# Kernel tuning notes

Measured on AMD Instinct MI355X. Metric: run time of the kernel, lower is better.

The kernel has to match this reference:

```python
import jax, jax.numpy as jnp
import numpy as np


def setup_inputs() -> dict:
    key = jax.random.key(0)
    ks = jax.random.split(key, 6)
    B, n_tok, n_RoI = 8, 64, 100
    T_hidden, I_hidden = 768, 1024
    P = I_hidden // 2  # projection = 512
    s_q = 1.0 / np.sqrt(T_hidden)
    s_k = 1.0 / np.sqrt(I_hidden)
    s_w = 1.0 / np.sqrt(P)
    return {
        "encT": jax.random.normal(ks[0], (B, n_tok, T_hidden), jnp.float32),
        "encI": jax.random.normal(ks[1], (B, n_RoI, I_hidden), jnp.float32),
        "mask": jnp.zeros((B, 1, n_tok, n_RoI), jnp.float32),
        "Wq": jax.random.normal(ks[2], (T_hidden, P), jnp.float32) * s_q,
        "bq": jnp.zeros((P,), jnp.float32),
        "Wk": jax.random.normal(ks[3], (I_hidden, P), jnp.float32) * s_k,
        "bk": jnp.zeros((P,), jnp.float32),
        "w": jax.random.normal(ks[4], (P,), jnp.float32) * s_w,
        "b": jnp.zeros((1,), jnp.float32),
    }


def reference(encT, encI, mask, Wq, bq, Wk, bk, w, b):
    # Q_mlp / K_mlp: Linear + exact GELU (torch nn.GELU default)
    q = jax.nn.gelu(jnp.einsum('bth,hp->btp', encT, Wq) + bq, approximate=False)  # [B,T,P]
    k = jax.nn.gelu(jnp.einsum('brh,hp->brp', encI, Wk) + bk, approximate=False)  # [B,R,P]
    # broadcast add (instead of repeat/view), tanh, then Linear(P,1)
    fusion = jnp.tanh(q[:, :, None, :] + k[:, None, :, :])  # [B,T,R,P]
    logits = jnp.einsum('btrp,p->btr', fusion, w) + b[0]      # [B,T,R]
    return logits + jnp.squeeze(mask, axis=1)
```

## Files before the change

### kernel.cpp

```cpp
#include <hip/hip_runtime.h>
#include <math.h>

#define B_  8
#define T_  64
#define R_  100
#define TH_ 768
#define IH_ 1024
#define P_  512
#define N_  512

#define CTANH 2.88539008177792681f

typedef short short8  __attribute__((ext_vector_type(8)));
typedef float floatx4 __attribute__((ext_vector_type(4)));

__device__ __forceinline__ ushort f2bf(float f) {
  union { float f; unsigned int u; } v; v.f = f;
  unsigned int r = v.u + 0x7FFFu + ((v.u >> 16) & 1u);
  return (ushort)(r >> 16);
}

#define PADK 40

__global__ __launch_bounds__(256) void mfma_linear_gelu(
    const float* __restrict__ encT, const float* __restrict__ Wq,
    const float* __restrict__ bq, float* __restrict__ qout,
    const float* __restrict__ encI, const float* __restrict__ Wk,
    const float* __restrict__ bk, float* __restrict__ kout) {
  const int rt = blockIdx.y;
  const bool isQ = rt < 8;
  const float* __restrict__ X = isQ ? encT : encI;
  const float* __restrict__ W = isQ ? Wq : Wk;
  const float* __restrict__ bias = isQ ? bq : bk;
  float* __restrict__ Y = isQ ? qout : kout;
  const int M    = isQ ? (B_ * T_) : (B_ * R_);
  const int KDIM = isQ ? TH_ : IH_;
  const int row0 = (isQ ? rt : (rt - 8)) * 64;
  const int col0 = blockIdx.x * 64;
  const int ntiles = KDIM / 32;

  __shared__ ushort As[64 * PADK];
  __shared__ ushort Bs[64 * PADK];

  const int tid = threadIdx.x;

  const int arow = tid >> 2;
  const int akq  = (tid & 3) * 8;
  const int arowc = min(row0 + arow, M - 1);
  const float* __restrict__ Xp = X + (size_t)arowc * KDIM + akq;

  const int bkp = (tid >> 4) * 2;
  const int bn4 = (tid & 15) * 4;
  const float* __restrict__ Wp = W + (size_t)bkp * N_ + col0 + bn4;

  const int wave = tid >> 6;
  const int lane = tid & 63;
  const int wm = (wave >> 1) * 32;
  const int wn = (wave & 1) * 32;
  const int l15 = lane & 15;
  const int q8  = (lane >> 4) * 8;

  floatx4 acc00 = {0.f,0.f,0.f,0.f}, acc01 = {0.f,0.f,0.f,0.f};
  floatx4 acc10 = {0.f,0.f,0.f,0.f}, acc11 = {0.f,0.f,0.f,0.f};

  float4 a0 = *(const float4*)(Xp + 0);
  float4 a1 = *(const float4*)(Xp + 4);
  float4 b0 = *(const float4*)(Wp);
  float4 b1 = *(const float4*)(Wp + N_);

  for (int kt = 0; kt < ntiles; ++kt) {
    {
      short8 pk;
      pk[0] = (short)f2bf(a0.x); pk[1] = (short)f2bf(a0.y);
      pk[2] = (short)f2bf(a0.z); pk[3] = (short)f2bf(a0.w);
      pk[4] = (short)f2bf(a1.x); pk[5] = (short)f2bf(a1.y);
      pk[6] = (short)f2bf(a1.z); pk[7] = (short)f2bf(a1.w);
      *(short8*)&As[arow * PADK + akq] = pk;
    }
    {
      unsigned int p0 = (unsigned int)f2bf(b0.x) | ((unsigned int)f2bf(b1.x) << 16);
      unsigned int p1 = (unsigned int)f2bf(b0.y) | ((unsigned int)f2bf(b1.y) << 16);
      unsigned int p2 = (unsigned int)f2bf(b0.z) | ((unsigned int)f2bf(b1.z) << 16);
      unsigned int p3 = (unsigned int)f2bf(b0.w) | ((unsigned int)f2bf(b1.w) << 16);
      *(unsigned int*)&Bs[(bn4 + 0) * PADK + bkp] = p0;
      *(unsigned int*)&Bs[(bn4 + 1) * PADK + bkp] = p1;
      *(unsigned int*)&Bs[(bn4 + 2) * PADK + bkp] = p2;
      *(unsigned int*)&Bs[(bn4 + 3) * PADK + bkp] = p3;
    }
    __syncthreads();

    if (kt + 1 < ntiles) {
      const int kb = (kt + 1) * 32;
      a0 = *(const float4*)(Xp + kb);
      a1 = *(const float4*)(Xp + kb + 4);
      b0 = *(const float4*)(W + (size_t)(kb + bkp) * N_ + col0 + bn4);
      b1 = *(const float4*)(W + (size_t)(kb + bkp + 1) * N_ + col0 + bn4);
    }

    short8 af0 = *(const short8*)&As[(wm + l15) * PADK + q8];
    short8 af1 = *(const short8*)&As[(wm + 16 + l15) * PADK + q8];
    short8 bf0 = *(const short8*)&Bs[(wn + l15) * PADK + q8];
    short8 bf1 = *(const short8*)&Bs[(wn + 16 + l15) * PADK + q8];
    acc00 = __builtin_amdgcn_mfma_f32_16x16x32_bf16(af0, bf0, acc00, 0, 0, 0);
    acc01 = __builtin_amdgcn_mfma_f32_16x16x32_bf16(af0, bf1, acc01, 0, 0, 0);
    acc10 = __builtin_amdgcn_mfma_f32_16x16x32_bf16(af1, bf0, acc10, 0, 0, 0);
    acc11 = __builtin_amdgcn_mfma_f32_16x16x32_bf16(af1, bf1, acc11, 0, 0, 0);
    __syncthreads();
  }

  const float is2 = 0.70710678118654752f;
  const float bia0 = bias[col0 + wn + l15];
  const float bia1 = bias[col0 + wn + 16 + l15];
  const int rbase = row0 + wm + (lane >> 4) * 4;

  #pragma unroll
  for (int r = 0; r < 4; ++r) {
    int row = rbase + r;
    if (row < M) {
      float v0 = acc00[r] + bia0;
      Y[(size_t)row * N_ + col0 + wn + l15] =
          CTANH * 0.5f * v0 * (1.f + erff(v0 * is2));
      float v1 = acc01[r] + bia1;
      Y[(size_t)row * N_ + col0 + wn + 16 + l15] =
          CTANH * 0.5f * v1 * (1.f + erff(v1 * is2));
    }
    int row2 = rbase + 16 + r;
    if (row2 < M) {
      float v2 = acc10[r] + bia0;
      Y[(size_t)row2 * N_ + col0 + wn + l15] =
          CTANH * 0.5f * v2 * (1.f + erff(v2 * is2));
      float v3 = acc11[r] + bia1;
      Y[(size_t)row2 * N_ + col0 + wn + 16 + l15] =
          CTANH * 0.5f * v3 * (1.f + erff(v3 * is2));
    }
  }
}

__global__ __launch_bounds__(256) void fuse_kernel(
    const float* __restrict__ q, const float* __restrict__ k,
    const float* __restrict__ w, const float* __restrict__ bscalar,
    const float* __restrict__ mask, float* __restrict__ out) {
  const int bt = blockIdx.x;
  const int wave = threadIdx.x >> 6;
  const int rg = blockIdx.y * 4 + wave;
  if (rg >= 25) return;
  const int lane = threadIdx.x & 63;
  const int sub  = lane >> 4;
  const int pi   = lane & 15;
  const int r = rg * 4 + sub;
  const int b = bt >> 6;

  const float* __restrict__ qp = q + (size_t)bt * P_ + pi * 4;
  const float* __restrict__ kp = k + (size_t)(b * R_ + r) * P_ + pi * 4;
  const float* __restrict__ wp = w + pi * 4;

  float acc0 = 0.f, acc1 = 0.f;
  #pragma unroll
  for (int i = 0; i < 8; ++i) {
    float4 qv = *(const float4*)(qp + i * 64);
    float4 kv = *(const float4*)(kp + i * 64);
    float4 wv = *(const float4*)(wp + i * 64);
    float x, e, d, s;
    x = qv.x + kv.x;
    e = __builtin_amdgcn_exp2f(x);
    d = __builtin_amdgcn_rcpf(1.f + e);
    s = fmaf(-2.f, d, 1.f);
    acc0 = fmaf(wv.x, s, acc0);
    x = qv.y + kv.y;
    e = __builtin_amdgcn_exp2f(x);
    d = __builtin_amdgcn_rcpf(1.f + e);
    s = fmaf(-2.f, d, 1.f);
    acc1 = fmaf(wv.y, s, acc1);
    x = qv.z + kv.z;
    e = __builtin_amdgcn_exp2f(x);
    d = __builtin_amdgcn_rcpf(1.f + e);
    s = fmaf(-2.f, d, 1.f);
    acc0 = fmaf(wv.z, s, acc0);
    x = qv.w + kv.w;
    e = __builtin_amdgcn_exp2f(x);
    d = __builtin_amdgcn_rcpf(1.f + e);
    s = fmaf(-2.f, d, 1.f);
    acc1 = fmaf(wv.w, s, acc1);
  }
  float acc = acc0 + acc1;
  #pragma unroll
  for (int off = 1; off < 16; off <<= 1) acc += __shfl_xor(acc, off, 64);

  if (pi == 0) {
    out[(size_t)bt * R_ + r] = acc + bscalar[0] + mask[(size_t)bt * R_ + r];
  }
}

extern "C" void kernel_launch(void* const* d_in, const int* in_sizes, int n_in,
                              void* d_out, int out_size, void* d_ws, size_t ws_size,
                              hipStream_t stream) {
  const float* encT = (const float*)d_in[0];
  const float* encI = (const float*)d_in[1];
  const float* mask = (const float*)d_in[2];
  const float* Wq   = (const float*)d_in[3];
  const float* bq   = (const float*)d_in[4];
  const float* Wk   = (const float*)d_in[5];
  const float* bk   = (const float*)d_in[6];
  const float* w    = (const float*)d_in[7];
  const float* bsc  = (const float*)d_in[8];
  float* out = (float*)d_out;

  float* q = (float*)d_ws;
  float* k = q + (size_t)B_ * T_ * P_;

  dim3 grid(N_ / 64, 8 + 13);
  mfma_linear_gelu<<<grid, 256, 0, stream>>>(encT, Wq, bq, q, encI, Wk, bk, k);

  fuse_kernel<<<dim3(512, 7), 256, 0, stream>>>(q, k, w, bsc, mask, out);
}
```

Baseline: 106.7 us.

## Split-K GEMM across four warp groups and store q/k in fp16

The linear+GELU GEMM now splits the K dimension across four 256-thread groups in a 1024-thread block, with a shared-memory tree reduction, and halves the column tile to 32 so more blocks are launched. The q/k intermediates are written as fp16, which halves the traffic into the fusion kernel. That kernel does the q+k add in half2 before the exp2/rcp tanh. The aim is better occupancy and parallelism in the small GEMM and less memory bandwidth in the fusion stage, at the cost of reduced precision for the pre-tanh sums and extra reduction synchronisation.

```diff
diff --git a/kernel.cpp b/kernel.cpp
--- a/kernel.cpp
+++ b/kernel.cpp
@@ -1,4 +1,5 @@
 #include <hip/hip_runtime.h>
+#include <hip/hip_fp16.h>
 #include <math.h>
 
 #define B_  8
@@ -22,51 +23,55 @@
 
 #define PADK 40
 
-__global__ __launch_bounds__(256) void mfma_linear_gelu(
+__global__ __launch_bounds__(1024) void mfma_linear_gelu_sk4(
     const float* __restrict__ encT, const float* __restrict__ Wq,
-    const float* __restrict__ bq, float* __restrict__ qout,
+    const float* __restrict__ bq, __half* __restrict__ qout,
     const float* __restrict__ encI, const float* __restrict__ Wk,
-    const float* __restrict__ bk, float* __restrict__ kout) {
+    const float* __restrict__ bk, __half* __restrict__ kout) {
   const int rt = blockIdx.y;
   const bool isQ = rt < 8;
   const float* __restrict__ X = isQ ? encT : encI;
   const float* __restrict__ W = isQ ? Wq : Wk;
   const float* __restrict__ bias = isQ ? bq : bk;
-  float* __restrict__ Y = isQ ? qout : kout;
+  __half* __restrict__ Y = isQ ? qout : kout;
   const int M    = isQ ? (B_ * T_) : (B_ * R_);
   const int KDIM = isQ ? TH_ : IH_;
   const int row0 = (isQ ? rt : (rt - 8)) * 64;
-  const int col0 = blockIdx.x * 64;
-  const int ntiles = KDIM / 32;
-
-  __shared__ ushort As[64 * PADK];
-  __shared__ ushort Bs[64 * PADK];
+  const int col0 = blockIdx.x * 32;
+  const int kq   = KDIM >> 2;
+  const int ntiles = kq / 32;
+
+  __shared__ ushort As[4][64 * PADK];
+  __shared__ ushort Bs[4][32 * PADK];
+  __shared__ float  red[2][64 * 33];
 
   const int tid = threadIdx.x;
-
-  const int arow = tid >> 2;
-  const int akq  = (tid & 3) * 8;
+  const int sp  = tid >> 8;
+  const int t   = tid & 255;
+  const int kbase = sp * kq;
+
+  const int arow = t >> 2;
+  const int akq  = (t & 3) * 8;
   const int arowc = min(row0 + arow, M - 1);
-  const float* __restrict__ Xp = X + (size_t)arowc * KDIM + akq;
-
-  const int bkp = (tid >> 4) * 2;
-  const int bn4 = (tid & 15) * 4;
-  const float* __restrict__ Wp = W + (size_t)bkp * N_ + col0 + bn4;
-
-  const int wave = tid >> 6;
-  const int lane = tid & 63;
-  const int wm = (wave >> 1) * 32;
-  const int wn = (wave & 1) * 32;
+  const float* __restrict__ Xp = X + (size_t)arowc * KDIM + kbase + akq;
+
+  const int bkp = (t >> 4) * 2;
+  const int bn2 = (t & 15) * 2;
+  const float* __restrict__ Wp = W + (size_t)(kbase + bkp) * N_ + col0 + bn2;
+
+  const int wv = t >> 6;
+  const int lane = t & 63;
+  const int wm = wv * 16;
   const int l15 = lane & 15;
   const int q8  = (lane >> 4) * 8;
-
-  floatx4 acc00 = {0.f,0.f,0.f,0.f}, acc01 = {0.f,0.f,0.f,0.f};
-  floatx4 acc10 = {0.f,0.f,0.f,0.f}, acc11 = {0.f,0.f,0.f,0.f};
-
-  float4 a0 = *(const float4*)(Xp + 0);
+  const int q4  = (lane >> 4) * 4;
+
+  floatx4 acc0 = {0.f,0.f,0.f,0.f}, acc1 = {0.f,0.f,0.f,0.f};
+
+  float4 a0 = *(const float4*)(Xp);
   float4 a1 = *(const float4*)(Xp + 4);
-  float4 b0 = *(const float4*)(Wp);
-  float4 b1 = *(const float4*)(Wp + N_);
+  float2 b0 = *(const float2*)(Wp);
+  float2 b1 = *(const float2*)(Wp + N_);
 
   for (int kt = 0; kt < ntiles; ++kt) {
     {
@@ -75,17 +80,13 @@
       pk[2] = (short)f2bf(a0.z); pk[3] = (short)f2bf(a0.w);
       pk[4] = (short)f2bf(a1.x); pk[5] = (short)f2bf(a1.y);
       pk[6] = (short)f2bf(a1.z); pk[7] = (short)f2bf(a1.w);
-      *(short8*)&As[arow * PADK + akq] = pk;
+      *(short8*)&As[sp][arow * PADK + akq] = pk;
     }
     {
       unsigned int p0 = (unsigned int)f2bf(b0.x) | ((unsigned int)f2bf(b1.x) << 16);
       unsigned int p1 = (unsigned int)f2bf(b0.y) | ((unsigned int)f2bf(b1.y) << 16);
-      unsigned int p2 = (unsigned int)f2bf(b0.z) | ((unsigned int)f2bf(b1.z) << 16);
-      unsigned int p3 = (unsigned int)f2bf(b0.w) | ((unsigned int)f2bf(b1.w) << 16);
-      *(unsigned int*)&Bs[(bn4 + 0) * PADK + bkp] = p0;
-      *(unsigned int*)&Bs[(bn4 + 1) * PADK + bkp] = p1;
-      *(unsigned int*)&Bs[(bn4 + 2) * PADK + bkp] = p2;
-      *(unsigned int*)&Bs[(bn4 + 3) * PADK + bkp] = p3;
+      *(unsigned int*)&Bs[sp][(bn2 + 0) * PADK + bkp] = p0;
+      *(unsigned int*)&Bs[sp][(bn2 + 1) * PADK + bkp] = p1;
     }
     __syncthreads();
 
@@ -93,51 +94,67 @@
       const int kb = (kt + 1) * 32;
       a0 = *(const float4*)(Xp + kb);
       a1 = *(const float4*)(Xp + kb + 4);
-      b0 = *(const float4*)(W + (size_t)(kb + bkp) * N_ + col0 + bn4);
-      b1 = *(const float4*)(W + (size_t)(kb + bkp + 1) * N_ + col0 + bn4);
-    }
-
-    short8 af0 = *(const short8*)&As[(wm + l15) * PADK + q8];
-    short8 af1 = *(const short8*)&As[(wm + 16 + l15) * PADK + q8];
-    short8 bf0 = *(const short8*)&Bs[(wn + l15) * PADK + q8];
-    short8 bf1 = *(const short8*)&Bs[(wn + 16 + l15) * PADK + q8];
-    acc00 = __builtin_amdgcn_mfma_f32_16x16x32_bf16(af0, bf0, acc00, 0, 0, 0);
-    acc01 = __builtin_amdgcn_mfma_f32_16x16x32_bf16(af0, bf1, acc01, 0, 0, 0);
-    acc10 = __builtin_amdgcn_mfma_f32_16x16x32_bf16(af1, bf0, acc10, 0, 0, 0);
-    acc11 = __builtin_amdgcn_mfma_f32_16x16x32_bf16(af1, bf1, acc11, 0, 0, 0);
+      b0 = *(const float2*)(Wp + (size_t)kb * N_);
+      b1 = *(const float2*)(Wp + (size_t)(kb + 1) * N_);
+    }
+
+    short8 af  = *(const short8*)&As[sp][(wm + l15) * PADK + q8];
+    short8 bf0 = *(const short8*)&Bs[sp][(l15) * PADK + q8];
+    short8 bf1 = *(const short8*)&Bs[sp][(16 + l15) * PADK + q8];
+    acc0 = __builtin_amdgcn_mfma_f32_16x16x32_bf16(af, bf0, acc0, 0, 0, 0);
+    acc1 = __builtin_amdgcn_mfma_f32_16x16x32_bf16(af, bf1, acc1, 0, 0, 0);
     __syncthreads();
   }
 
-  const float is2 = 0.70710678118654752f;
-  const float bia0 = bias[col0 + wn + l15];
-  const float bia1 = bias[col0 + wn + 16 + l15];
-  const int rbase = row0 + wm + (lane >> 4) * 4;
-
-  #pragma unroll
-  for (int r = 0; r < 4; ++r) {
-    int row = rbase + r;
-    if (row < M) {
-      float v0 = acc00[r] + bia0;
-      Y[(size_t)row * N_ + col0 + wn + l15] =
-          CTANH * 0.5f * v0 * (1.f + erff(v0 * is2));
-      float v1 = acc01[r] + bia1;
-      Y[(size_t)row * N_ + col0 + wn + 16 + l15] =
-          CTANH * 0.5f * v1 * (1.f + erff(v1 * is2));
-    }
-    int row2 = rbase + 16 + r;
-    if (row2 < M) {
-      float v2 = acc10[r] + bia0;
-      Y[(size_t)row2 * N_ + col0 + wn + l15] =
-          CTANH * 0.5f * v2 * (1.f + erff(v2 * is2));
-      float v3 = acc11[r] + bia1;
-      Y[(size_t)row2 * N_ + col0 + wn + 16 + l15] =
-          CTANH * 0.5f * v3 * (1.f + erff(v3 * is2));
-    }
-  }
-}
-
-__global__ __launch_bounds__(256) void fuse_kernel(
-    const float* __restrict__ q, const float* __restrict__ k,
+  if (sp >= 2) {
+    float* L = red[sp - 2];
+    #pragma unroll
+    for (int j = 0; j < 4; ++j) {
+      L[(wm + q4 + j) * 33 + l15]      = acc0[j];
+      L[(wm + q4 + j) * 33 + 16 + l15] = acc1[j];
+    }
+  }
+  __syncthreads();
+  if (sp < 2) {
+    const float* L = red[sp];
+    #pragma unroll
+    for (int j = 0; j < 4; ++j) {
+      acc0[j] += L[(wm + q4 + j) * 33 + l15];
+      acc1[j] += L[(wm + q4 + j) * 33 + 16 + l15];
+    }
+  }
+  __syncthreads();
+  if (sp == 1) {
+    float* L = red[0];
+    #pragma unroll
+    for (int j = 0; j < 4; ++j) {
+      L[(wm + q4 + j) * 33 + l15]      = acc0[j];
+      L[(wm + q4 + j) * 33 + 16 + l15] = acc1[j];
+    }
+  }
+  __syncthreads();
+  if (sp == 0) {
+    const float* L = red[0];
+    const float is2 = 0.70710678118654752f;
+    const float bia0 = bias[col0 + l15];
+    const float bia1 = bias[col0 + 16 + l15];
+    #pragma unroll
+    for (int j = 0; j < 4; ++j) {
+      const int row = row0 + wm + q4 + j;
+      if (row < M) {
+        float v0 = acc0[j] + L[(wm + q4 + j) * 33 + l15] + bia0;
+        float v1 = acc1[j] + L[(wm + q4 + j) * 33 + 16 + l15] + bia1;
+        v0 = CTANH * 0.5f * v0 * (1.f + erff(v0 * is2));
+        v1 = CTANH * 0.5f * v1 * (1.f + erff(v1 * is2));
+        Y[(size_t)row * N_ + col0 + l15]      = __float2half(v0);
+        Y[(size_t)row * N_ + col0 + 16 + l15] = __float2half(v1);
+      }
+    }
+  }
+}
+
+__global__ __launch_bounds__(256) void fuse_kernel_h(
+    const __half* __restrict__ q, const __half* __restrict__ k,
     const float* __restrict__ w, const float* __restrict__ bscalar,
     const float* __restrict__ mask, float* __restrict__ out) {
   const int bt = blockIdx.x;
@@ -150,37 +167,32 @@
   const int r = rg * 4 + sub;
   const int b = bt >> 6;
 
-  const float* __restrict__ qp = q + (size_t)bt * P_ + pi * 4;
-  const float* __restrict__ kp = k + (size_t)(b * R_ + r) * P_ + pi * 4;
-  const float* __restrict__ wp = w + pi * 4;
+  const __half* __restrict__ qp = q + (size_t)bt * P_ + pi * 8;
+  const __half* __restrict__ kp = k + (size_t)(b * R_ + r) * P_ + pi * 8;
+  const float* __restrict__ wp = w + pi * 8;
 
   float acc0 = 0.f, acc1 = 0.f;
   #pragma unroll
-  for (int i = 0; i < 8; ++i) {
-    float4 qv = *(const float4*)(qp + i * 64);
-    float4 kv = *(const float4*)(kp + i * 64);
-    float4 wv = *(const float4*)(wp + i * 64);
-    float x, e, d, s;
-    x = qv.x + kv.x;
-    e = __builtin_amdgcn_exp2f(x);
-    d = __builtin_amdgcn_rcpf(1.f + e);
-    s = fmaf(-2.f, d, 1.f);
-    acc0 = fmaf(wv.x, s, acc0);
-    x = qv.y + kv.y;
-    e = __builtin_amdgcn_exp2f(x);
-    d = __builtin_amdgcn_rcpf(1.f + e);
-    s = fmaf(-2.f, d, 1.f);
-    acc1 = fmaf(wv.y, s, acc1);
-    x = qv.z + kv.z;
-    e = __builtin_amdgcn_exp2f(x);
-    d = __builtin_amdgcn_rcpf(1.f + e);
-    s = fmaf(-2.f, d, 1.f);
-    acc0 = fmaf(wv.z, s, acc0);
-    x = qv.w + kv.w;
-    e = __builtin_amdgcn_exp2f(x);
-    d = __builtin_amdgcn_rcpf(1.f + e);
-    s = fmaf(-2.f, d, 1.f);
-    acc1 = fmaf(wv.w, s, acc1);
+  for (int i = 0; i < 4; ++i) {
+    union { float4 f; __half2 h[4]; } qu, ku;
+    qu.f = *(const float4*)(qp + i * 128);
+    ku.f = *(const float4*)(kp + i * 128);
+    float4 w0 = *(const float4*)(wp + i * 128);
+    float4 w1 = *(const float4*)(wp + i * 128 + 4);
+    #pragma unroll
+    for (int e = 0; e < 4; ++e) {
+      __half2 s = __hadd2(qu.h[e], ku.h[e]);
+      float x0 = __low2float(s);
+      float x1 = __high2float(s);
+      float d0 = __builtin_amdgcn_rcpf(1.f + __builtin_amdgcn_exp2f(x0));
+      float d1 = __builtin_amdgcn_rcpf(1.f + __builtin_amdgcn_exp2f(x1));
+      float s0 = fmaf(-2.f, d0, 1.f);
+      float s1 = fmaf(-2.f, d1, 1.f);
+      const float we0 = (e == 0) ? w0.x : (e == 1) ? w0.z : (e == 2) ? w1.x : w1.z;
+      const float we1 = (e == 0) ? w0.y : (e == 1) ? w0.w : (e == 2) ? w1.y : w1.w;
+      acc0 = fmaf(we0, s0, acc0);
+      acc1 = fmaf(we1, s1, acc1);
+    }
   }
   float acc = acc0 + acc1;
   #pragma unroll
@@ -205,11 +217,12 @@
   const float* bsc  = (const float*)d_in[8];
   float* out = (float*)d_out;
 
-  float* q = (float*)d_ws;
-  float* k = q + (size_t)B_ * T_ * P_;
-
-  dim3 grid(N_ / 64, 8 + 13);
-  mfma_linear_gelu<<<grid, 256, 0, stream>>>(encT, Wq, bq, q, encI, Wk, bk, k);
-
-  fuse_kernel<<<dim3(512, 7), 256, 0, stream>>>(q, k, w, bsc, mask, out);
-}
+  __half* q = (__half*)d_ws;
+  __half* k = q + (size_t)B_ * T_ * P_;
+
+  dim3 grid(N_ / 32, 8 + 13);
+  mfma_linear_gelu_sk4<<<grid, 1024, 0, stream>>>(encT, Wq, bq, q,
+                                                  encI, Wk, bk, k);
+
+  fuse_kernel_h<<<dim3(512, 7), 256, 0, stream>>>(q, k, w, bsc, mask, out);
+}
```

Measured after the change: 95.86 us. 10.2% less time.
